# Kernel optimization log

Hardware: AMD Instinct MI355X
Metric: run time of the kernel (lower is better)

Reference implementation:

```python
import jax, jax.numpy as jnp
import numpy as np

T, H, I, E, K = 4096, 2048, 2048, 16, 4
EPS = 1e-6


def setup_inputs() -> dict:
    key = jax.random.key(0)
    ks = jax.random.split(key, 7)
    s = 0.02
    return {
        "x": jax.random.normal(ks[0], (T, H), dtype=jnp.float32),
        "gamma": jnp.ones((H,), dtype=jnp.float32),
        "wg": jax.random.normal(ks[1], (E, H), dtype=jnp.float32) * s,
        "bg": jax.random.normal(ks[2], (E,), dtype=jnp.float32) * s,
        "w1": jax.random.normal(ks[3], (E, I, H), dtype=jnp.float32) * s,  # gate proj
        "w3": jax.random.normal(ks[4], (E, I, H), dtype=jnp.float32) * s,  # up proj
        "w2": jax.random.normal(ks[5], (E, H, I), dtype=jnp.float32) * s,  # down proj
    }


def reference(x, gamma, wg, bg, w1, w3, w2):
    # RMSNorm
    t = x * jax.lax.rsqrt(jnp.mean(x * x, axis=-1, keepdims=True) + EPS) * gamma
    # Router: softmax -> top-k -> renormalize (FusedMoE renormalize=True)
    logits = t @ wg.T + bg                        # [T, E]
    probs = jax.nn.softmax(logits, axis=-1)
    vals, idx = jax.lax.top_k(probs, K)           # [T, K]
    vals = vals / jnp.sum(vals, axis=-1, keepdims=True)
    # Dense [T, E] routing-weight matrix (zeros outside top-k)
    route_w = jnp.einsum("tk,tke->te", vals, jax.nn.one_hot(idx, E, dtype=vals.dtype))
    # Grouped expert GEMMs: scan over experts, accumulate weighted outputs
    def body(acc, p):
        w1e, w3e, w2e, we = p                     # [I,H], [I,H], [H,I], [T]
        h = jax.nn.silu(t @ w1e.T) * (t @ w3e.T)  # [T, I]
        return acc + (h @ w2e.T) * we[:, None], None
    moe_out, _ = jax.lax.scan(body, jnp.zeros_like(x), (w1, w3, w2, route_w.T))
    return x + moe_out
```

## Files before the change

kernel.cpp:

```cpp
#include <hip/hip_runtime.h>
#include <hip/hip_bf16.h>

constexpr int TT = 4096;
constexpr int HH = 2048;
constexpr int II = 2048;
constexpr int EE = 16;
constexpr int KTOP = 4;

typedef __attribute__((ext_vector_type(4))) float f4;
typedef __attribute__((ext_vector_type(8))) short s8;
typedef __attribute__((ext_vector_type(4))) short sh4;

__device__ __forceinline__ short f2bf(float f) {
    union { __hip_bfloat16 b; short s; } u;
    u.b = __float2bfloat16(f);
    return u.s;
}
__device__ __forceinline__ float bf2f(short s) {
    union { unsigned u; float f; } v;
    v.u = ((unsigned)(unsigned short)s) << 16;
    return v.f;
}

__global__ void k_router(const float* __restrict__ x, const float* __restrict__ gamma,
                         const float* __restrict__ wg, const float* __restrict__ bg,
                         short* __restrict__ t16, int* __restrict__ cnt,
                         int* __restrict__ lst, float* __restrict__ lwt) {
    const int tok = blockIdx.x;
    const int lane = threadIdx.x & 63;
    const int w = threadIdx.x >> 6;

    const f4* xr = (const f4*)(x + (size_t)tok * HH);
    const f4* gr = (const f4*)gamma;

    f4 t4[8];
    float ss = 0.f;
#pragma unroll
    for (int j = 0; j < 8; j++) {
        f4 v = xr[lane + 64 * j];
        t4[j] = v;
        ss += v[0] * v[0] + v[1] * v[1] + v[2] * v[2] + v[3] * v[3];
    }
#pragma unroll
    for (int m = 32; m >= 1; m >>= 1) ss += __shfl_xor(ss, m);
    const float rs = rsqrtf(ss * (1.f / HH) + 1e-6f);
#pragma unroll
    for (int j = 0; j < 8; j++) {
        f4 g = gr[lane + 64 * j];
#pragma unroll
        for (int i = 0; i < 4; i++) t4[j][i] *= rs * g[i];
    }

    if (w == 0) {
        short* tr = t16 + (size_t)tok * HH;
#pragma unroll
        for (int j = 0; j < 8; j++) {
            sh4 o;
#pragma unroll
            for (int i = 0; i < 4; i++) o[i] = f2bf(t4[j][i]);
            *(sh4*)(tr + (size_t)(lane + 64 * j) * 4) = o;
        }
    }

    __shared__ float sh_logit[EE];
#pragma unroll
    for (int q = 0; q < 4; q++) {
        const int e = w * 4 + q;
        const f4* wrow = (const f4*)(wg + (size_t)e * HH);
        float a = 0.f;
#pragma unroll
        for (int j = 0; j < 8; j++) {
            f4 wv = wrow[lane + 64 * j];
            a += t4[j][0] * wv[0] + t4[j][1] * wv[1] + t4[j][2] * wv[2] + t4[j][3] * wv[3];
        }
#pragma unroll
        for (int m = 32; m >= 1; m >>= 1) a += __shfl_xor(a, m);
        if (lane == 0) sh_logit[e] = a + bg[e];
    }
    __syncthreads();

    if (threadIdx.x == 0) {
        float logit[EE];
#pragma unroll
        for (int e = 0; e < EE; e++) logit[e] = sh_logit[e];
        unsigned chosen = 0u;
        int sel[KTOP]; float sv[KTOP];
#pragma unroll
        for (int k = 0; k < KTOP; k++) {
            float best = -1e30f; int bi = 0;
#pragma unroll
            for (int e = 0; e < EE; e++) {
                bool take = (!((chosen >> e) & 1u)) && (logit[e] > best);
                if (take) { best = logit[e]; bi = e; }
            }
            chosen |= 1u << bi; sel[k] = bi; sv[k] = best;
        }
        const float lmax = sv[0];
        float s = 0.f;
#pragma unroll
        for (int k = 0; k < KTOP; k++) { sv[k] = expf(sv[k] - lmax); s += sv[k]; }
        const float inv = 1.f / s;
#pragma unroll
        for (int k = 0; k < KTOP; k++) {
            int e = sel[k];
            int p = atomicAdd(&cnt[e], 1);
            lst[e * TT + p] = tok * KTOP + k;
            lwt[e * TT + p] = sv[k] * inv;
        }
    }
}

__global__ __launch_bounds__(256, 2) void k_gemm_ffn_fused(
        const short* __restrict__ t16, const float* __restrict__ w1,
        const float* __restrict__ w3, short* __restrict__ h,
        const int* __restrict__ cnt, const int* __restrict__ lst) {
    const int e = blockIdx.z;
    const int Me = cnt[e];
    const int m0 = blockIdx.y * 128;
    if (m0 >= Me) return;
    const int n0 = blockIdx.x * 128;
    const float* we1 = w1 + (size_t)e * II * HH;
    const float* we3 = w3 + (size_t)e * II * HH;

    __shared__ char lA[16384];
    __shared__ char lB1[16384];
    __shared__ char lB2[16384];
    __shared__ int s_tok[128];

    const int tid = threadIdx.x;
    if (tid < 128) s_tok[tid] = (m0 + tid < Me) ? lst[e * TT + m0 + tid] : 0;
    __syncthreads();

    const int lane = tid & 63, wid = tid >> 6;
    const int wr = wid >> 1, wc = wid & 1;

    f4 acc1[4][4], acc2[4][4];
    const f4 zero = {0.f, 0.f, 0.f, 0.f};
#pragma unroll
    for (int i = 0; i < 4; i++)
#pragma unroll
        for (int j = 0; j < 4; j++) { acc1[i][j] = zero; acc2[i][j] = zero; }

    const int rbase = tid >> 3;
    const int kc = (tid & 7) * 8;
    const int lb0 = rbase * 128 + ((kc * 2) ^ ((rbase & 7) << 4));
    int tokrow[4];
#pragma unroll
    for (int j = 0; j < 4; j++) tokrow[j] = s_tok[rbase + 32 * j] >> 2;

    for (int kt = 0; kt < HH / 64; ++kt) {
        __syncthreads();
#pragma unroll
        for (int j = 0; j < 4; j++) {
            s8 av = *(const s8*)(t16 + (size_t)tokrow[j] * HH + kt * 64 + kc);
            *(s8*)(lA + lb0 + 4096 * j) = av;
        }
#pragma unroll
        for (int j = 0; j < 4; j++) {
            size_t roff = (size_t)(n0 + rbase + 32 * j) * HH + kt * 64 + kc;
            {
                f4 b0 = *(const f4*)(we1 + roff);
                f4 b1 = *(const f4*)(we1 + roff + 4);
                s8 bv;
#pragma unroll
                for (int i = 0; i < 4; i++) { bv[i] = f2bf(b0[i]); bv[4 + i] = f2bf(b1[i]); }
                *(s8*)(lB1 + lb0 + 4096 * j) = bv;
            }
            {
                f4 b0 = *(const f4*)(we3 + roff);
                f4 b1 = *(const f4*)(we3 + roff + 4);
                s8 bv;
#pragma unroll
                for (int i = 0; i < 4; i++) { bv[i] = f2bf(b0[i]); bv[4 + i] = f2bf(b1[i]); }
                *(s8*)(lB2 + lb0 + 4096 * j) = bv;
            }
        }
        __syncthreads();
#pragma unroll
        for (int kk = 0; kk < 2; ++kk) {
            s8 af[4], b1v[4], b2v[4];
#pragma unroll
            for (int mf = 0; mf < 4; mf++) {
                int r = wr * 64 + mf * 16 + (lane & 15);
                int byte = r * 128 + (((kk * 64) + ((lane >> 4) << 4)) ^ ((r & 7) << 4));
                af[mf] = *(const s8*)(lA + byte);
            }
#pragma unroll
            for (int nf = 0; nf < 4; nf++) {
                int r = wc * 64 + nf * 16 + (lane & 15);
                int byte = r * 128 + (((kk * 64) + ((lane >> 4) << 4)) ^ ((r & 7) << 4));
                b1v[nf] = *(const s8*)(lB1 + byte);
                b2v[nf] = *(const s8*)(lB2 + byte);
            }
#pragma unroll
            for (int mf = 0; mf < 4; mf++)
#pragma unroll
                for (int nf = 0; nf < 4; nf++) {
                    acc1[mf][nf] = __builtin_amdgcn_mfma_f32_16x16x32_bf16(
                        af[mf], b1v[nf], acc1[mf][nf], 0, 0, 0);
                    acc2[mf][nf] = __builtin_amdgcn_mfma_f32_16x16x32_bf16(
                        af[mf], b2v[nf], acc2[mf][nf], 0, 0, 0);
                }
        }
    }
#pragma unroll
    for (int mf = 0; mf < 4; mf++) {
#pragma unroll
        for (int j = 0; j < 4; j++) {
            int rl = wr * 64 + mf * 16 + ((lane >> 4) << 2) + j;
            if (m0 + rl < Me) {
                size_t orow = (size_t)s_tok[rl] * II;
#pragma unroll
                for (int nf = 0; nf < 4; nf++) {
                    int ncol = n0 + wc * 64 + nf * 16 + (lane & 15);
                    float g = acc1[mf][nf][j];
                    float u = acc2[mf][nf][j];
                    float sg = g / (1.f + expf(-g));
                    h[orow + ncol] = f2bf(sg * u);
                }
            }
        }
    }
}

__global__ __launch_bounds__(256, 2) void k_gemm_down(
        const short* __restrict__ h, const float* __restrict__ w2,
        short* __restrict__ buf2, const int* __restrict__ cnt,
        const int* __restrict__ lst, const float* __restrict__ lwt) {
    const int e = blockIdx.z;
    const int Me = cnt[e];
    const int m0 = blockIdx.y * 128;
    if (m0 >= Me) return;
    const int n0 = blockIdx.x * 128;
    const float* we = w2 + (size_t)e * HH * II;

    __shared__ char lA[16384];
    __shared__ char lB[16384];
    __shared__ int s_tok[128];
    __shared__ float s_wgt[128];

    const int tid = threadIdx.x;
    if (tid < 128) {
        bool v = (m0 + tid < Me);
        s_tok[tid] = v ? lst[e * TT + m0 + tid] : 0;
        s_wgt[tid] = v ? lwt[e * TT + m0 + tid] : 0.f;
    }
    __syncthreads();

    const int lane = tid & 63, wid = tid >> 6;
    const int wr = wid >> 1, wc = wid & 1;

    f4 acc[4][4];
    const f4 zero = {0.f, 0.f, 0.f, 0.f};
#pragma unroll
    for (int i = 0; i < 4; i++)
#pragma unroll
        for (int j = 0; j < 4; j++) acc[i][j] = zero;

    const int rbase = tid >> 3;
    const int kc = (tid & 7) * 8;
    const int lb0 = rbase * 128 + ((kc * 2) ^ ((rbase & 7) << 4));
    const short* gA[4]; const float* gB[4];
#pragma unroll
    for (int j = 0; j < 4; j++) {
        gA[j] = h + (size_t)s_tok[rbase + 32 * j] * II + kc;
        gB[j] = we + (size_t)(n0 + rbase + 32 * j) * II + kc;
    }

    s8 ar[4]; f4 br[4][2];
#define PREFETCH(kt)                                                           \
    _Pragma("unroll")                                                          \
    for (int j = 0; j < 4; j++) {                                              \
        ar[j] = *(const s8*)(gA[j] + (kt) * 64);                               \
        br[j][0] = *(const f4*)(gB[j] + (kt) * 64);                            \
        br[j][1] = *(const f4*)(gB[j] + (kt) * 64 + 4);                        \
    }

    PREFETCH(0);
    const int nkt = II / 64;
    for (int kt = 0; kt < nkt; ++kt) {
        asm volatile("" ::: "memory");
        __builtin_amdgcn_s_barrier();
        asm volatile("" ::: "memory");
#pragma unroll
        for (int j = 0; j < 4; j++) {
            *(s8*)(lA + lb0 + 4096 * j) = ar[j];
            s8 bv;
#pragma unroll
            for (int i = 0; i < 4; i++) { bv[i] = f2bf(br[j][0][i]); bv[4 + i] = f2bf(br[j][1][i]); }
            *(s8*)(lB + lb0 + 4096 * j) = bv;
        }
        if (kt + 1 < nkt) PREFETCH(kt + 1);
        asm volatile("s_waitcnt lgkmcnt(0)" ::: "memory");
        __builtin_amdgcn_s_barrier();
        asm volatile("" ::: "memory");
#pragma unroll
        for (int kk = 0; kk < 2; ++kk) {
            s8 af[4], bfr[4];
#pragma unroll
            for (int mf = 0; mf < 4; mf++) {
                int r = wr * 64 + mf * 16 + (lane & 15);
                int byte = r * 128 + (((kk * 64) + ((lane >> 4) << 4)) ^ ((r & 7) << 4));
                af[mf] = *(const s8*)(lA + byte);
            }
#pragma unroll
            for (int nf = 0; nf < 4; nf++) {
                int r = wc * 64 + nf * 16 + (lane & 15);
                int byte = r * 128 + (((kk * 64) + ((lane >> 4) << 4)) ^ ((r & 7) << 4));
                bfr[nf] = *(const s8*)(lB + byte);
            }
#pragma unroll
            for (int mf = 0; mf < 4; mf++)
#pragma unroll
                for (int nf = 0; nf < 4; nf++)
                    acc[mf][nf] = __builtin_amdgcn_mfma_f32_16x16x32_bf16(
                        af[mf], bfr[nf], acc[mf][nf], 0, 0, 0);
        }
    }
#undef PREFETCH
#pragma unroll
    for (int mf = 0; mf < 4; mf++) {
#pragma unroll
        for (int j = 0; j < 4; j++) {
            int rl = wr * 64 + mf * 16 + ((lane >> 4) << 2) + j;
            if (m0 + rl < Me) {
                size_t orow = (size_t)s_tok[rl] * HH;
                float wgt = s_wgt[rl];
#pragma unroll
                for (int nf = 0; nf < 4; nf++) {
                    int ncol = n0 + wc * 64 + nf * 16 + (lane & 15);
                    buf2[orow + ncol] = f2bf(acc[mf][nf][j] * wgt);
                }
            }
        }
    }
}

__global__ void k_final(const float* __restrict__ x, const short* __restrict__ buf2,
                        float* __restrict__ out) {
    size_t i8 = (size_t)blockIdx.x * 256 + threadIdx.x;
    size_t tok = i8 / (HH / 8);
    size_t c8 = i8 % (HH / 8);
    const f4* xp = (const f4*)x + i8 * 2;
    f4 r0 = xp[0], r1 = xp[1];
#pragma unroll
    for (int k = 0; k < KTOP; k++) {
        s8 b = ((const s8*)buf2)[(tok * KTOP + k) * (HH / 8) + c8];
#pragma unroll
        for (int j = 0; j < 4; j++) { r0[j] += bf2f(b[j]); r1[j] += bf2f(b[4 + j]); }
    }
    ((f4*)out)[i8 * 2] = r0;
    ((f4*)out)[i8 * 2 + 1] = r1;
}

extern "C" void kernel_launch(void* const* d_in, const int* in_sizes, int n_in,
                              void* d_out, int out_size, void* d_ws, size_t ws_size,
                              hipStream_t stream) {
    const float* x     = (const float*)d_in[0];
    const float* gamma = (const float*)d_in[1];
    const float* wg    = (const float*)d_in[2];
    const float* bg    = (const float*)d_in[3];
    const float* w1    = (const float*)d_in[4];
    const float* w3    = (const float*)d_in[5];
    const float* w2    = (const float*)d_in[6];
    float* out = (float*)d_out;

    char* ws = (char*)d_ws;
    size_t off = 0;
    short* t16  = (short*)(ws + off); off += (size_t)TT * HH * 2;
    short* h1   = (short*)(ws + off); off += (size_t)TT * KTOP * II * 2;
    short* buf2 = (short*)(ws + off); off += (size_t)TT * KTOP * HH * 2;
    int* cnt    = (int*)(ws + off); off += 256;
    int* lst    = (int*)(ws + off); off += (size_t)EE * TT * 4;
    float* lwt  = (float*)(ws + off); off += (size_t)EE * TT * 4;

    hipMemsetAsync(cnt, 0, EE * sizeof(int), stream);
    k_router<<<TT, 256, 0, stream>>>(x, gamma, wg, bg, t16, cnt, lst, lwt);

    dim3 g1(II / 128, TT / 128, EE);
    k_gemm_ffn_fused<<<g1, 256, 0, stream>>>(t16, w1, w3, h1, cnt, lst);

    dim3 g2(HH / 128, TT / 128, EE);
    k_gemm_down<<<g2, 256, 0, stream>>>(h1, w2, buf2, cnt, lst, lwt);

    k_final<<<(TT * HH / 8) / 256, 256, 0, stream>>>(x, buf2, out);
}
```

Before: 906.1 us.

## Widen down-proj GEMM tile to 128x256 and drop register prefetch

The down-projection kernel now computes a 128x256 output tile per block, doubling the N extent, the B shared-memory buffer and the per-wave accumulators. Each gathered A tile of h is reused across twice as many output columns, halving A reloads and the launched block count. The register double-buffered prefetch is replaced by direct load-then-store with plain __syncthreads. This exposes global load latency and raises register pressure (128 accumulator floats per thread) under launch_bounds(256,2), which risks spills or lower occupancy.

```diff
diff --git a/kernel.cpp b/kernel.cpp
--- a/kernel.cpp
+++ b/kernel.cpp
@@ -231,11 +231,11 @@
     const int Me = cnt[e];
     const int m0 = blockIdx.y * 128;
     if (m0 >= Me) return;
-    const int n0 = blockIdx.x * 128;
+    const int n0 = blockIdx.x * 256;
     const float* we = w2 + (size_t)e * HH * II;
 
     __shared__ char lA[16384];
-    __shared__ char lB[16384];
+    __shared__ char lB[32768];
     __shared__ int s_tok[128];
     __shared__ float s_wgt[128];
 
@@ -250,53 +250,41 @@
     const int lane = tid & 63, wid = tid >> 6;
     const int wr = wid >> 1, wc = wid & 1;
 
-    f4 acc[4][4];
+    f4 acc[4][8];
     const f4 zero = {0.f, 0.f, 0.f, 0.f};
 #pragma unroll
     for (int i = 0; i < 4; i++)
 #pragma unroll
-        for (int j = 0; j < 4; j++) acc[i][j] = zero;
+        for (int j = 0; j < 8; j++) acc[i][j] = zero;
 
     const int rbase = tid >> 3;
     const int kc = (tid & 7) * 8;
     const int lb0 = rbase * 128 + ((kc * 2) ^ ((rbase & 7) << 4));
-    const short* gA[4]; const float* gB[4];
-#pragma unroll
-    for (int j = 0; j < 4; j++) {
-        gA[j] = h + (size_t)s_tok[rbase + 32 * j] * II + kc;
-        gB[j] = we + (size_t)(n0 + rbase + 32 * j) * II + kc;
-    }
-
-    s8 ar[4]; f4 br[4][2];
-#define PREFETCH(kt)                                                           \
-    _Pragma("unroll")                                                          \
-    for (int j = 0; j < 4; j++) {                                              \
-        ar[j] = *(const s8*)(gA[j] + (kt) * 64);                               \
-        br[j][0] = *(const f4*)(gB[j] + (kt) * 64);                            \
-        br[j][1] = *(const f4*)(gB[j] + (kt) * 64 + 4);                        \
-    }
-
-    PREFETCH(0);
-    const int nkt = II / 64;
-    for (int kt = 0; kt < nkt; ++kt) {
-        asm volatile("" ::: "memory");
-        __builtin_amdgcn_s_barrier();
-        asm volatile("" ::: "memory");
-#pragma unroll
-        for (int j = 0; j < 4; j++) {
-            *(s8*)(lA + lb0 + 4096 * j) = ar[j];
+    int arow[4];
+#pragma unroll
+    for (int j = 0; j < 4; j++) arow[j] = s_tok[rbase + 32 * j];
+
+    for (int kt = 0; kt < II / 64; ++kt) {
+        __syncthreads();
+#pragma unroll
+        for (int j = 0; j < 4; j++) {
+            s8 av = *(const s8*)(h + (size_t)arow[j] * II + kt * 64 + kc);
+            *(s8*)(lA + lb0 + 4096 * j) = av;
+        }
+#pragma unroll
+        for (int j = 0; j < 8; j++) {
+            const float* gp = we + (size_t)(n0 + rbase + 32 * j) * II + kt * 64 + kc;
+            f4 b0 = *(const f4*)gp;
+            f4 b1 = *(const f4*)(gp + 4);
             s8 bv;
 #pragma unroll
-            for (int i = 0; i < 4; i++) { bv[i] = f2bf(br[j][0][i]); bv[4 + i] = f2bf(br[j][1][i]); }
+            for (int i = 0; i < 4; i++) { bv[i] = f2bf(b0[i]); bv[4 + i] = f2bf(b1[i]); }
             *(s8*)(lB + lb0 + 4096 * j) = bv;
         }
-        if (kt + 1 < nkt) PREFETCH(kt + 1);
-        asm volatile("s_waitcnt lgkmcnt(0)" ::: "memory");
-        __builtin_amdgcn_s_barrier();
-        asm volatile("" ::: "memory");
+        __syncthreads();
 #pragma unroll
         for (int kk = 0; kk < 2; ++kk) {
-            s8 af[4], bfr[4];
+            s8 af[4], bfr[8];
 #pragma unroll
             for (int mf = 0; mf < 4; mf++) {
                 int r = wr * 64 + mf * 16 + (lane & 15);
@@ -304,20 +292,19 @@
                 af[mf] = *(const s8*)(lA + byte);
             }
 #pragma unroll
-            for (int nf = 0; nf < 4; nf++) {
-                int r = wc * 64 + nf * 16 + (lane & 15);
+            for (int nf = 0; nf < 8; nf++) {
+                int r = wc * 128 + nf * 16 + (lane & 15);
                 int byte = r * 128 + (((kk * 64) + ((lane >> 4) << 4)) ^ ((r & 7) << 4));
                 bfr[nf] = *(const s8*)(lB + byte);
             }
 #pragma unroll
             for (int mf = 0; mf < 4; mf++)
 #pragma unroll
-                for (int nf = 0; nf < 4; nf++)
+                for (int nf = 0; nf < 8; nf++)
                     acc[mf][nf] = __builtin_amdgcn_mfma_f32_16x16x32_bf16(
                         af[mf], bfr[nf], acc[mf][nf], 0, 0, 0);
         }
     }
-#undef PREFETCH
 #pragma unroll
     for (int mf = 0; mf < 4; mf++) {
 #pragma unroll
@@ -327,8 +314,8 @@
                 size_t orow = (size_t)s_tok[rl] * HH;
                 float wgt = s_wgt[rl];
 #pragma unroll
-                for (int nf = 0; nf < 4; nf++) {
-                    int ncol = n0 + wc * 64 + nf * 16 + (lane & 15);
+                for (int nf = 0; nf < 8; nf++) {
+                    int ncol = n0 + wc * 128 + nf * 16 + (lane & 15);
                     buf2[orow + ncol] = f2bf(acc[mf][nf][j] * wgt);
                 }
             }
@@ -380,7 +367,7 @@
     dim3 g1(II / 128, TT / 128, EE);
     k_gemm_ffn_fused<<<g1, 256, 0, stream>>>(t16, w1, w3, h1, cnt, lst);
 
-    dim3 g2(HH / 128, TT / 128, EE);
+    dim3 g2(HH / 256, TT / 128, EE);
     k_gemm_down<<<g2, 256, 0, stream>>>(h1, w2, buf2, cnt, lst, lwt);
 
     k_final<<<(TT * HH / 8) / 256, 256, 0, stream>>>(x, buf2, out);
```

Result: slower. 945.9 us (+4.4%).

## Pre-convert down-proj weights to bf16 and use 256x256 double-buffered direct-to-LDS GEMM

Applied to the files above, without the earlier changes.

Adds a separate pass that converts w2 to bf16 in the workspace on every call. The down-projection GEMM is rewritten with 256x256 tiles and 512 threads, using global_load_lds async copies into double-buffered LDS, with s_setprio around the MFMA block. This removes the in-loop fp32-to-bf16 conversion and register staging, and raises reuse per tile. The cost is an extra full read/write pass over w2 (about 256MB read), more LDS use, and fewer tail blocks. The final kernel is also changed to a grid-stride loop over 2048 blocks.

```diff
diff --git a/kernel.cpp b/kernel.cpp
--- a/kernel.cpp
+++ b/kernel.cpp
@@ -20,6 +20,12 @@
     union { unsigned u; float f; } v;
     v.u = ((unsigned)(unsigned short)s) << 16;
     return v.f;
+}
+
+__device__ __forceinline__ void g2l16(const void* g, void* l) {
+    __builtin_amdgcn_global_load_lds(
+        (const __attribute__((address_space(1))) void*)g,
+        (__attribute__((address_space(3))) void*)l, 16, 0, 0);
 }
 
 __global__ void k_router(const float* __restrict__ x, const float* __restrict__ gamma,
@@ -108,6 +114,16 @@
             lwt[e * TT + p] = sv[k] * inv;
         }
     }
+}
+
+__global__ void k_convert(const float* __restrict__ src, short* __restrict__ dst) {
+    size_t i = (size_t)blockIdx.x * 256 + threadIdx.x;
+    f4 a = ((const f4*)src)[i * 2];
+    f4 b = ((const f4*)src)[i * 2 + 1];
+    s8 o;
+#pragma unroll
+    for (int j = 0; j < 4; j++) { o[j] = f2bf(a[j]); o[4 + j] = f2bf(b[j]); }
+    ((s8*)dst)[i] = o;
 }
 
 __global__ __launch_bounds__(256, 2) void k_gemm_ffn_fused(
@@ -223,112 +239,116 @@
     }
 }
 
-__global__ __launch_bounds__(256, 2) void k_gemm_down(
-        const short* __restrict__ h, const float* __restrict__ w2,
+__global__ __launch_bounds__(512, 2) void k_down256(
+        const short* __restrict__ h, const short* __restrict__ w2b,
         short* __restrict__ buf2, const int* __restrict__ cnt,
         const int* __restrict__ lst, const float* __restrict__ lwt) {
     const int e = blockIdx.z;
     const int Me = cnt[e];
-    const int m0 = blockIdx.y * 128;
+    const int m0 = blockIdx.y * 256;
     if (m0 >= Me) return;
-    const int n0 = blockIdx.x * 128;
-    const float* we = w2 + (size_t)e * HH * II;
-
-    __shared__ char lA[16384];
-    __shared__ char lB[16384];
-    __shared__ int s_tok[128];
-    __shared__ float s_wgt[128];
+    const int n0 = blockIdx.x * 256;
+    const short* we = w2b + (size_t)e * HH * II;
+
+    __shared__ short lA[2][256 * 64];
+    __shared__ short lB[2][256 * 64];
+    __shared__ int s_tok[256];
+    __shared__ float s_wgt[256];
 
     const int tid = threadIdx.x;
-    if (tid < 128) {
+    if (tid < 256) {
         bool v = (m0 + tid < Me);
         s_tok[tid] = v ? lst[e * TT + m0 + tid] : 0;
         s_wgt[tid] = v ? lwt[e * TT + m0 + tid] : 0.f;
     }
     __syncthreads();
 
-    const int lane = tid & 63, wid = tid >> 6;
-    const int wr = wid >> 1, wc = wid & 1;
-
-    f4 acc[4][4];
+    const int lane = tid & 63, w = tid >> 6;
+    const int wr = w >> 2, wcol = w & 3;
+
+    const short* ga[4]; const short* gb[4];
+    {
+        const int rsub = tid >> 3;
+        const int csw = ((tid & 7) ^ (rsub & 7)) * 8;
+#pragma unroll
+        for (int i = 0; i < 4; i++) {
+            int row = i * 64 + rsub;
+            ga[i] = h + (size_t)s_tok[row] * II + csw;
+            gb[i] = we + (size_t)(n0 + row) * II + csw;
+        }
+    }
+
+    f4 acc[8][4];
     const f4 zero = {0.f, 0.f, 0.f, 0.f};
 #pragma unroll
-    for (int i = 0; i < 4; i++)
+    for (int i = 0; i < 8; i++)
 #pragma unroll
         for (int j = 0; j < 4; j++) acc[i][j] = zero;
 
-    const int rbase = tid >> 3;
-    const int kc = (tid & 7) * 8;
-    const int lb0 = rbase * 128 + ((kc * 2) ^ ((rbase & 7) << 4));
-    const short* gA[4]; const float* gB[4];
-#pragma unroll
-    for (int j = 0; j < 4; j++) {
-        gA[j] = h + (size_t)s_tok[rbase + 32 * j] * II + kc;
-        gB[j] = we + (size_t)(n0 + rbase + 32 * j) * II + kc;
-    }
-
-    s8 ar[4]; f4 br[4][2];
-#define PREFETCH(kt)                                                           \
-    _Pragma("unroll")                                                          \
-    for (int j = 0; j < 4; j++) {                                              \
-        ar[j] = *(const s8*)(gA[j] + (kt) * 64);                               \
-        br[j][0] = *(const f4*)(gB[j] + (kt) * 64);                            \
-        br[j][1] = *(const f4*)(gB[j] + (kt) * 64 + 4);                        \
-    }
-
-    PREFETCH(0);
+#define STG(db, kt)                                                            \
+    {                                                                          \
+        _Pragma("unroll")                                                      \
+        for (int i = 0; i < 4; i++)                                            \
+            g2l16(ga[i] + (kt) * 64, (char*)lA[db] + i * 8192 + w * 1024);     \
+        _Pragma("unroll")                                                      \
+        for (int i = 0; i < 4; i++)                                            \
+            g2l16(gb[i] + (kt) * 64, (char*)lB[db] + i * 8192 + w * 1024);     \
+    }
+
+    STG(0, 0);
+    asm volatile("s_waitcnt vmcnt(0)" ::: "memory");
+    __builtin_amdgcn_s_barrier();
+    asm volatile("" ::: "memory");
+
     const int nkt = II / 64;
+    int cur = 0;
     for (int kt = 0; kt < nkt; ++kt) {
+        if (kt + 1 < nkt) STG(cur ^ 1, kt + 1);
+
+#pragma unroll
+        for (int kk = 0; kk < 2; ++kk) {
+            s8 af[8], bf[4];
+#pragma unroll
+            for (int mf = 0; mf < 8; mf++) {
+                int r = wr * 128 + mf * 16 + (lane & 15);
+                int off = (kk * 64 + ((lane >> 4) << 4)) ^ ((r & 7) << 4);
+                af[mf] = *(const s8*)((const char*)lA[cur] + r * 128 + off);
+            }
+#pragma unroll
+            for (int nf = 0; nf < 4; nf++) {
+                int r = wcol * 64 + nf * 16 + (lane & 15);
+                int off = (kk * 64 + ((lane >> 4) << 4)) ^ ((r & 7) << 4);
+                bf[nf] = *(const s8*)((const char*)lB[cur] + r * 128 + off);
+            }
+            __builtin_amdgcn_s_setprio(1);
+#pragma unroll
+            for (int mf = 0; mf < 8; mf++)
+#pragma unroll
+                for (int nf = 0; nf < 4; nf++)
+                    acc[mf][nf] = __builtin_amdgcn_mfma_f32_16x16x32_bf16(
+                        af[mf], bf[nf], acc[mf][nf], 0, 0, 0);
+            __builtin_amdgcn_s_setprio(0);
+        }
+
+        asm volatile("s_waitcnt vmcnt(0)" ::: "memory");
         asm volatile("" ::: "memory");
         __builtin_amdgcn_s_barrier();
         asm volatile("" ::: "memory");
+        cur ^= 1;
+    }
+#undef STG
+
+#pragma unroll
+    for (int mf = 0; mf < 8; mf++) {
 #pragma unroll
         for (int j = 0; j < 4; j++) {
-            *(s8*)(lA + lb0 + 4096 * j) = ar[j];
-            s8 bv;
-#pragma unroll
-            for (int i = 0; i < 4; i++) { bv[i] = f2bf(br[j][0][i]); bv[4 + i] = f2bf(br[j][1][i]); }
-            *(s8*)(lB + lb0 + 4096 * j) = bv;
-        }
-        if (kt + 1 < nkt) PREFETCH(kt + 1);
-        asm volatile("s_waitcnt lgkmcnt(0)" ::: "memory");
-        __builtin_amdgcn_s_barrier();
-        asm volatile("" ::: "memory");
-#pragma unroll
-        for (int kk = 0; kk < 2; ++kk) {
-            s8 af[4], bfr[4];
-#pragma unroll
-            for (int mf = 0; mf < 4; mf++) {
-                int r = wr * 64 + mf * 16 + (lane & 15);
-                int byte = r * 128 + (((kk * 64) + ((lane >> 4) << 4)) ^ ((r & 7) << 4));
-                af[mf] = *(const s8*)(lA + byte);
-            }
-#pragma unroll
-            for (int nf = 0; nf < 4; nf++) {
-                int r = wc * 64 + nf * 16 + (lane & 15);
-                int byte = r * 128 + (((kk * 64) + ((lane >> 4) << 4)) ^ ((r & 7) << 4));
-                bfr[nf] = *(const s8*)(lB + byte);
-            }
-#pragma unroll
-            for (int mf = 0; mf < 4; mf++)
-#pragma unroll
-                for (int nf = 0; nf < 4; nf++)
-                    acc[mf][nf] = __builtin_amdgcn_mfma_f32_16x16x32_bf16(
-                        af[mf], bfr[nf], acc[mf][nf], 0, 0, 0);
-        }
-    }
-#undef PREFETCH
-#pragma unroll
-    for (int mf = 0; mf < 4; mf++) {
-#pragma unroll
-        for (int j = 0; j < 4; j++) {
-            int rl = wr * 64 + mf * 16 + ((lane >> 4) << 2) + j;
+            int rl = wr * 128 + mf * 16 + ((lane >> 4) << 2) + j;
             if (m0 + rl < Me) {
                 size_t orow = (size_t)s_tok[rl] * HH;
                 float wgt = s_wgt[rl];
 #pragma unroll
                 for (int nf = 0; nf < 4; nf++) {
-                    int ncol = n0 + wc * 64 + nf * 16 + (lane & 15);
+                    int ncol = n0 + wcol * 64 + nf * 16 + (lane & 15);
                     buf2[orow + ncol] = f2bf(acc[mf][nf][j] * wgt);
                 }
             }
@@ -338,19 +358,22 @@
 
 __global__ void k_final(const float* __restrict__ x, const short* __restrict__ buf2,
                         float* __restrict__ out) {
-    size_t i8 = (size_t)blockIdx.x * 256 + threadIdx.x;
-    size_t tok = i8 / (HH / 8);
-    size_t c8 = i8 % (HH / 8);
-    const f4* xp = (const f4*)x + i8 * 2;
-    f4 r0 = xp[0], r1 = xp[1];
-#pragma unroll
-    for (int k = 0; k < KTOP; k++) {
-        s8 b = ((const s8*)buf2)[(tok * KTOP + k) * (HH / 8) + c8];
-#pragma unroll
-        for (int j = 0; j < 4; j++) { r0[j] += bf2f(b[j]); r1[j] += bf2f(b[4 + j]); }
-    }
-    ((f4*)out)[i8 * 2] = r0;
-    ((f4*)out)[i8 * 2 + 1] = r1;
+    const size_t total = (size_t)TT * HH / 8;
+    for (size_t i8 = (size_t)blockIdx.x * 256 + threadIdx.x; i8 < total;
+         i8 += (size_t)gridDim.x * 256) {
+        size_t tok = i8 / (HH / 8);
+        size_t c8 = i8 % (HH / 8);
+        const f4* xp = (const f4*)x + i8 * 2;
+        f4 r0 = xp[0], r1 = xp[1];
+#pragma unroll
+        for (int k = 0; k < KTOP; k++) {
+            s8 b = ((const s8*)buf2)[(tok * KTOP + k) * (HH / 8) + c8];
+#pragma unroll
+            for (int j = 0; j < 4; j++) { r0[j] += bf2f(b[j]); r1[j] += bf2f(b[4 + j]); }
+        }
+        ((f4*)out)[i8 * 2] = r0;
+        ((f4*)out)[i8 * 2 + 1] = r1;
+    }
 }
 
 extern "C" void kernel_launch(void* const* d_in, const int* in_sizes, int n_in,
@@ -370,6 +393,7 @@
     short* t16  = (short*)(ws + off); off += (size_t)TT * HH * 2;
     short* h1   = (short*)(ws + off); off += (size_t)TT * KTOP * II * 2;
     short* buf2 = (short*)(ws + off); off += (size_t)TT * KTOP * HH * 2;
+    short* wbuf = (short*)(ws + off); off += (size_t)EE * HH * II * 2;
     int* cnt    = (int*)(ws + off); off += 256;
     int* lst    = (int*)(ws + off); off += (size_t)EE * TT * 4;
     float* lwt  = (float*)(ws + off); off += (size_t)EE * TT * 4;
@@ -377,11 +401,14 @@
     hipMemsetAsync(cnt, 0, EE * sizeof(int), stream);
     k_router<<<TT, 256, 0, stream>>>(x, gamma, wg, bg, t16, cnt, lst, lwt);
 
+    const int convBlocks = (EE * HH * II / 8) / 256;
+    k_convert<<<convBlocks, 256, 0, stream>>>(w2, wbuf);
+
     dim3 g1(II / 128, TT / 128, EE);
     k_gemm_ffn_fused<<<g1, 256, 0, stream>>>(t16, w1, w3, h1, cnt, lst);
 
-    dim3 g2(HH / 128, TT / 128, EE);
-    k_gemm_down<<<g2, 256, 0, stream>>>(h1, w2, buf2, cnt, lst, lwt);
-
-    k_final<<<(TT * HH / 8) / 256, 256, 0, stream>>>(x, buf2, out);
-}
+    dim3 g2(HH / 256, TT / 256, EE);
+    k_down256<<<g2, 512, 0, stream>>>(h1, wbuf, buf2, cnt, lst, lwt);
+
+    k_final<<<2048, 256, 0, stream>>>(x, buf2, out);
+}
```

New measurement: 977.1 us. 1.08x slower.
